# Performance work log

Hardware: AMD Instinct MI355X
Metric: run time of the kernel (lower is better)

Reference implementation:

```python
import jax, jax.numpy as jnp
import numpy as np

N_NODES = 100000

def _gcn_norm(edge_index, num_nodes):
    # PyG GCNConv: add self-loops, symmetric normalization deg^-1/2 A_hat deg^-1/2
    loop = jnp.arange(num_nodes, dtype=edge_index.dtype)
    src = jnp.concatenate([edge_index[0], loop])  # [E+N]
    dst = jnp.concatenate([edge_index[1], loop])  # [E+N]
    deg = jax.ops.segment_sum(jnp.ones(dst.shape[0], jnp.float32), dst, num_segments=num_nodes)
    dis = jnp.where(deg > 0, jax.lax.rsqrt(deg), 0.0)
    norm = dis[src] * dis[dst]  # [E+N]
    return src, dst, norm

def _gcn_layer(x, W, b, src, dst, norm, num_nodes):
    xw = x @ W                                   # [N, H] dense GEMM first (out_dim <= in_dim)
    msg = xw[src] * norm[:, None]                # gather + scale per edge
    out = jax.ops.segment_sum(msg, dst, num_segments=num_nodes)  # scatter-add
    return out + b

def setup_inputs() -> dict:
    key = jax.random.key(0)
    ks = jax.random.split(key, 6)
    E = 1600000
    return {
        "x": jax.random.normal(ks[0], (N_NODES, 512), jnp.float32),
        "edge_index": jax.random.randint(ks[1], (2, E), 0, N_NODES, dtype=jnp.int64),
        "W1": jax.random.normal(ks[2], (512, 256), jnp.float32) * 0.04,
        "b1": jnp.zeros((256,), jnp.float32),
        "W2": jax.random.normal(ks[3], (256, 256), jnp.float32) * 0.06,
        "b2": jnp.zeros((256,), jnp.float32),
        "fc_w": jax.random.normal(ks[4], (256, 128), jnp.float32) * 0.06,
        "fc_b": jnp.zeros((128,), jnp.float32),
    }

def reference(x, edge_index, W1, b1, W2, b2, fc_w, fc_b):
    src, dst, norm = _gcn_norm(edge_index, N_NODES)
    h = jax.nn.relu(_gcn_layer(x, W1, b1, src, dst, norm, N_NODES))
    h = jax.nn.relu(_gcn_layer(h, W2, b2, src, dst, norm, N_NODES))
    return h @ fc_w + fc_b
```

## Files before the change

### kernel.cpp

```cpp
#include <hip/hip_runtime.h>


#define N_NODES 100000
constexpr int D_IN  = 512;
constexpr int D_H   = 256;
constexpr int D_OUT = 128;
constexpr int M_PAD = 100096;

typedef _Float16 f16x8 __attribute__((ext_vector_type(8)));
typedef _Float16 f16x4 __attribute__((ext_vector_type(4)));
typedef float f32x4 __attribute__((ext_vector_type(4)));

#define GLD16(SRC, DST) __builtin_amdgcn_global_load_lds(                      \
    (const __attribute__((address_space(1))) void*)(SRC),                      \
    (__attribute__((address_space(3))) void*)(DST), 16, 0, 0)

__global__ __launch_bounds__(256) void cvt_x_k(const float* __restrict__ x,
                                               _Float16* __restrict__ x16) {
  size_t i = ((size_t)blockIdx.x * 256 + threadIdx.x) * 8;
  const size_t valid = (size_t)N_NODES * D_IN;
  if (i < valid) {
    float4 a = *(const float4*)(x + i);
    float4 b = *(const float4*)(x + i + 4);
    f16x8 v;
    v[0] = (_Float16)a.x; v[1] = (_Float16)a.y;
    v[2] = (_Float16)a.z; v[3] = (_Float16)a.w;
    v[4] = (_Float16)b.x; v[5] = (_Float16)b.y;
    v[6] = (_Float16)b.z; v[7] = (_Float16)b.w;
    *(f16x8*)(x16 + i) = v;
  } else if (i < (size_t)M_PAD * D_IN) {
    *(f16x8*)(x16 + i) = (f16x8){0, 0, 0, 0, 0, 0, 0, 0};
  }
}

__global__ __launch_bounds__(256) void deg_count_k(const int* __restrict__ dst,
                                                   int* __restrict__ deg,
                                                   int* __restrict__ pe, int E) {
  int i = (blockIdx.x * 256 + threadIdx.x) * 4;
  if (i + 3 < E) {
    int4 d = *(const int4*)(dst + i);
    int4 p;
    p.x = atomicAdd(&deg[d.x], 1);
    p.y = atomicAdd(&deg[d.y], 1);
    p.z = atomicAdd(&deg[d.z], 1);
    p.w = atomicAdd(&deg[d.w], 1);
    *(int4*)(pe + i) = p;
  } else {
    for (int t = i; t < E; ++t) pe[t] = atomicAdd(&deg[dst[t]], 1);
  }
}

__global__ __launch_bounds__(256) void scan1_k(const int* __restrict__ deg,
                                               int* __restrict__ off,
                                               int* __restrict__ bsum,
                                               float* __restrict__ dis, int n) {
  __shared__ int ts[256];
  const int tid = threadIdx.x;
  const int base = blockIdx.x * 1024 + tid * 4;
  int v[4];
#pragma unroll
  for (int t = 0; t < 4; ++t) v[t] = (base + t < n) ? deg[base + t] : 0;
#pragma unroll
  for (int t = 0; t < 4; ++t)
    if (base + t < n) dis[base + t] = rsqrtf((float)v[t] + 1.0f);
  const int tot = v[0] + v[1] + v[2] + v[3];
  ts[tid] = tot;
  __syncthreads();
  for (int o = 1; o < 256; o <<= 1) {
    int t = (tid >= o) ? ts[tid - o] : 0;
    __syncthreads();
    ts[tid] += t;
    __syncthreads();
  }
  int run = ts[tid] - tot;
#pragma unroll
  for (int t = 0; t < 4; ++t) {
    if (base + t < n) off[base + t] = run;
    run += v[t];
  }
  if (tid == 255) bsum[blockIdx.x] = ts[255];
}

__global__ __launch_bounds__(128) void scan2_k(int* __restrict__ bsum, int nb) {
  __shared__ int ts[128];
  const int tid = threadIdx.x;
  const int v = (tid < nb) ? bsum[tid] : 0;
  ts[tid] = v;
  __syncthreads();
  for (int o = 1; o < 128; o <<= 1) {
    int t = (tid >= o) ? ts[tid - o] : 0;
    __syncthreads();
    ts[tid] += t;
    __syncthreads();
  }
  if (tid < nb) bsum[tid] = ts[tid] - v;
}

__global__ __launch_bounds__(256) void fill_k(const int* __restrict__ src,
                                              const int* __restrict__ dst,
                                              const int* __restrict__ pe,
                                              const int* __restrict__ off,
                                              const int* __restrict__ bsum,
                                              int* __restrict__ ssorted, int E) {
  int i = (blockIdx.x * 256 + threadIdx.x) * 4;
  if (i + 3 < E) {
    int4 s = *(const int4*)(src + i);
    int4 d = *(const int4*)(dst + i);
    int4 p = *(const int4*)(pe + i);
    ssorted[off[d.x] + bsum[d.x >> 10] + p.x] = s.x;
    ssorted[off[d.y] + bsum[d.y >> 10] + p.y] = s.y;
    ssorted[off[d.z] + bsum[d.z >> 10] + p.z] = s.z;
    ssorted[off[d.w] + bsum[d.w >> 10] + p.w] = s.w;
  } else {
    for (int t = i; t < E; ++t) {
      int d = dst[t];
      ssorted[off[d] + bsum[d >> 10] + pe[t]] = src[t];
    }
  }
}

__global__ __launch_bounds__(256) void wtrans_all_k(const float* __restrict__ W1,
                                                    const float* __restrict__ W2,
                                                    const float* __restrict__ FC,
                                                    _Float16* __restrict__ w1t,
                                                    _Float16* __restrict__ w2t,
                                                    _Float16* __restrict__ fct) {
  int i = blockIdx.x * 256 + threadIdx.x;
  if (i < 131072) {
    int k = i >> 8, n = i & 255;
    w1t[(size_t)n * 512 + k] = (_Float16)W1[i];
  } else if (i < 196608) {
    int j = i - 131072;
    int k = j >> 8, n = j & 255;
    w2t[(size_t)n * 256 + k] = (_Float16)W2[j];
  } else if (i < 229376) {
    int j = i - 196608;
    int k = j >> 7, n = j & 127;
    fct[(size_t)n * 256 + k] = (_Float16)FC[j];
  }
}

template<int BN, bool OUT_Y>
__global__ __launch_bounds__(512, 4) void gemm_glds_k(
    const _Float16* __restrict__ A16,
    const _Float16* __restrict__ Bt,
    const float* __restrict__ bias,
    const float* __restrict__ dis,
    float* __restrict__ C,
    _Float16* __restrict__ Y,
    int M, int K) {
  constexpr int BM = 128, BK = 32;
  constexpr int FN  = BN / 64;
  constexpr int NBI = BN / 128;
  constexpr int ASZ = BM * BK;
  constexpr int BSZ = BN * BK;
  constexpr int EPAD = 4;

  __shared__ __align__(16) _Float16 smem[3 * (ASZ + BSZ)];
  _Float16* As = smem;
  _Float16* Bs = smem + 3 * ASZ;
  float* epi = (float*)smem;

  const int tid  = threadIdx.x;
  const int w    = tid >> 6, lane = tid & 63;
  const int wm   = w >> 2, wn = w & 3;
  const int l15  = lane & 15, l16 = lane >> 4;
  const int row0 = blockIdx.y * BM;

  const int lr = lane >> 2, lg = lane & 3;
  const int arow  = w * 16 + lr;
  const int brow0 = w * (NBI * 16) + lr;
  const int brow1 = brow0 + 16;
  const _Float16* srcA  = A16 + (size_t)(row0 + arow) * K + ((lg ^ (arow & 3)) << 3);
  const _Float16* srcB0 = Bt + (size_t)brow0 * K + ((lg ^ (brow0 & 3)) << 3);
  const _Float16* srcB1 = Bt + (size_t)brow1 * K + ((lg ^ (brow1 & 3)) << 3);
  _Float16* dstA  = &As[(w * 16) * BK];
  _Float16* dstB0 = &Bs[(w * (NBI * 16)) * BK];
  _Float16* dstB1 = &Bs[(w * (NBI * 16) + 16) * BK];

  f32x4 acc[4][FN];
#pragma unroll
  for (int i = 0; i < 4; ++i)
#pragma unroll
    for (int j = 0; j < FN; ++j) acc[i][j] = (f32x4){0.f, 0.f, 0.f, 0.f};

  const int nsteps = K >> 5;

  auto stage = [&](int t, int buf) {
    const int kt = t << 5;
    GLD16(srcA + kt, dstA + buf * ASZ);
    GLD16(srcB0 + kt, dstB0 + buf * BSZ);
    if constexpr (NBI == 2) GLD16(srcB1 + kt, dstB1 + buf * BSZ);
  };

  stage(0, 0);
  if (nsteps > 1) stage(1, 1);

  int rbuf = 0;
  int wbuf = 2;
  for (int t = 0; t < nsteps; ++t) {
    if (t + 1 < nsteps) {
      if constexpr (NBI == 2) asm volatile("s_waitcnt vmcnt(3)" ::: "memory");
      else                    asm volatile("s_waitcnt vmcnt(2)" ::: "memory");
    } else {
      asm volatile("s_waitcnt vmcnt(0)" ::: "memory");
    }
    __builtin_amdgcn_sched_barrier(0);
    __builtin_amdgcn_s_barrier();
    __builtin_amdgcn_sched_barrier(0);

    if (t + 2 < nsteps) stage(t + 2, wbuf);

    const _Float16* as = As + rbuf * ASZ;
    const _Float16* bs = Bs + rbuf * BSZ;
    f16x8 a[4], b[FN];
#pragma unroll
    for (int i = 0; i < 4; ++i) {
      const int r = wm * 64 + i * 16 + l15;
      a[i] = *(const f16x8*)&as[r * BK + ((l16 ^ (r & 3)) << 3)];
    }
#pragma unroll
    for (int j = 0; j < FN; ++j) {
      const int n = wn * (FN * 16) + j * 16 + l15;
      b[j] = *(const f16x8*)&bs[n * BK + ((l16 ^ (n & 3)) << 3)];
    }
#pragma unroll
    for (int i = 0; i < 4; ++i)
#pragma unroll
      for (int j = 0; j < FN; ++j)
        acc[i][j] = __builtin_amdgcn_mfma_f32_16x16x32_f16(a[i], b[j], acc[i][j], 0, 0, 0);

    rbuf = (rbuf == 2) ? 0 : rbuf + 1;
    wbuf = (wbuf == 2) ? 0 : wbuf + 1;
  }
  __syncthreads();

  constexpr int ESTR = BN + EPAD;
  constexpr int CPT  = BN / 16;
#pragma unroll
  for (int c = 0; c < 4; ++c) {
    if (wm == (c >> 1)) {
      const int ib = (c & 1) * 2;
#pragma unroll
      for (int ii = 0; ii < 2; ++ii) {
        const int i = ib + ii;
#pragma unroll
        for (int j = 0; j < FN; ++j) {
          const int col = wn * (FN * 16) + j * 16 + l15;
#pragma unroll
          for (int r = 0; r < 4; ++r) {
            const int lrow = ii * 16 + l16 * 4 + r;
            epi[lrow * ESTR + col] = acc[i][j][r];
          }
        }
      }
    }
    __syncthreads();
    {
      const int lrow = tid >> 4;
      const int grow = row0 + c * 32 + lrow;
      const int colb = (tid & 15) * CPT;
      if (grow < M) {
        float v[CPT];
#pragma unroll
        for (int q = 0; q < CPT; q += 4)
          *(float4*)&v[q] = *(const float4*)&epi[lrow * ESTR + colb + q];
        if constexpr (OUT_Y) {
          const float dv = dis[grow];
          f16x8 o[CPT / 8];
#pragma unroll
          for (int q = 0; q < CPT; ++q) o[q >> 3][q & 7] = (_Float16)(v[q] * dv);
#pragma unroll
          for (int q = 0; q < CPT / 8; ++q)
            *(f16x8*)(Y + (size_t)grow * BN + colb + q * 8) = o[q];
        } else {
#pragma unroll
          for (int q = 0; q < CPT; ++q) v[q] += bias[colb + q];
#pragma unroll
          for (int q = 0; q < CPT; q += 4)
            *(float4*)(C + (size_t)grow * BN + colb + q) = *(const float4*)&v[q];
        }
      }
    }
    __syncthreads();
  }
}

__global__ __launch_bounds__(256) void gather_k(const _Float16* __restrict__ y,
                                                const int* __restrict__ ssorted,
                                                const int* __restrict__ off,
                                                const int* __restrict__ bsum,
                                                const float* __restrict__ dis,
                                                const float* __restrict__ bias,
                                                _Float16* __restrict__ h,
                                                int n, int E) {
  const int gid = blockIdx.x * 256 + threadIdx.x;
  const int v = gid >> 6, lane = gid & 63;
  if (v >= n) return;

  const float dv = dis[v];
  const int fo = lane * 4;

  f16x4 sv = *(const f16x4*)(y + (size_t)v * 256 + fo);
  float4 acc = make_float4((float)sv[0], (float)sv[1], (float)sv[2], (float)sv[3]);

  const int beg = off[v] + bsum[v >> 10];
  const int end = (v + 1 < n) ? (off[v + 1] + bsum[(v + 1) >> 10]) : E;
  const int ne = end - beg;

  for (int j0 = 0; j0 < ne; j0 += 64) {
    const int rem = ne - j0;
    const int cnt = rem < 64 ? rem : 64;
    int s_l = 0;
    if (lane < cnt) s_l = ssorted[beg + j0 + lane];

    int k = 0;
    for (; k + 8 <= cnt; k += 8) {
      f16x4 yv[8];
#pragma unroll
      for (int u = 0; u < 8; ++u) {
        const int s = __shfl(s_l, k + u);
        yv[u] = *(const f16x4*)(y + (size_t)s * 256 + fo);
      }
#pragma unroll
      for (int u = 0; u < 8; ++u) {
        acc.x += (float)yv[u][0];
        acc.y += (float)yv[u][1];
        acc.z += (float)yv[u][2];
        acc.w += (float)yv[u][3];
      }
    }
    for (; k < cnt; ++k) {
      const int s = __shfl(s_l, k);
      const f16x4 yv = *(const f16x4*)(y + (size_t)s * 256 + fo);
      acc.x += (float)yv[0];
      acc.y += (float)yv[1];
      acc.z += (float)yv[2];
      acc.w += (float)yv[3];
    }
  }

  const float4 b = *(const float4*)(bias + fo);
  f16x4 o;
  o[0] = (_Float16)fmaxf(fmaf(dv, acc.x, b.x), 0.f);
  o[1] = (_Float16)fmaxf(fmaf(dv, acc.y, b.y), 0.f);
  o[2] = (_Float16)fmaxf(fmaf(dv, acc.z, b.z), 0.f);
  o[3] = (_Float16)fmaxf(fmaf(dv, acc.w, b.w), 0.f);
  *(f16x4*)(h + (size_t)v * 256 + fo) = o;
}

extern "C" void kernel_launch(void* const* d_in, const int* in_sizes, int n_in,
                              void* d_out, int out_size, void* d_ws, size_t ws_size,
                              hipStream_t stream) {
  const float* x    = (const float*)d_in[0];
  const int*   ei   = (const int*)d_in[1];
  const float* W1   = (const float*)d_in[2];
  const float* b1   = (const float*)d_in[3];
  const float* W2   = (const float*)d_in[4];
  const float* b2   = (const float*)d_in[5];
  const float* fc_w = (const float*)d_in[6];
  const float* fc_b = (const float*)d_in[7];
  float* out = (float*)d_out;

  const int E = in_sizes[1] / 2;
  const int* src = ei;
  const int* dst = ei + E;
  const int N = N_NODES;

  char* p = (char*)d_ws;
  int*   deg     = (int*)p;            p += (size_t)N * 4;
  float* dis     = (float*)p;          p += (size_t)N * 4;
  int*   off     = (int*)p;            p += (size_t)(N + 1) * 4;
  int*   pe      = (int*)p;            p += (size_t)E * 4;
  int*   ssorted = (int*)p;            p += (size_t)E * 4;
  int*   bsum    = (int*)p;            p += 512;
  p = (char*)(((size_t)p + 255) & ~(size_t)255);
  _Float16* w1t = (_Float16*)p;        p += (size_t)D_H   * D_IN * 2;
  _Float16* w2t = (_Float16*)p;        p += (size_t)D_H   * D_H  * 2;
  _Float16* fct = (_Float16*)p;        p += (size_t)D_OUT * D_H  * 2;
  p = (char*)(((size_t)p + 255) & ~(size_t)255);
  _Float16* x16 = (_Float16*)p;        p += (size_t)M_PAD * D_IN * 2;
  _Float16* y16 = (_Float16*)p;        p += (size_t)M_PAD * D_H * 2;
  _Float16* h16 = (_Float16*)p;        p += (size_t)M_PAD * D_H * 2;

  cvt_x_k<<<(M_PAD * (D_IN / 8) + 255) / 256, 256, 0, stream>>>(x, x16);
  wtrans_all_k<<<896, 256, 0, stream>>>(W1, W2, fc_w, w1t, w2t, fct);

  const int NB1 = (N + 1023) / 1024;
  const int EB4 = ((E + 3) / 4 + 255) / 256;
  hipMemsetAsync(deg, 0, N * sizeof(int), stream);
  deg_count_k<<<EB4, 256, 0, stream>>>(dst, deg, pe, E);
  scan1_k<<<NB1, 256, 0, stream>>>(deg, off, bsum, dis, N);
  scan2_k<<<1, 128, 0, stream>>>(bsum, NB1);
  fill_k<<<EB4, 256, 0, stream>>>(src, dst, pe, off, bsum, ssorted, E);

  const int node_wave_blocks = (N * 64 + 255) / 256;
  const dim3 gg(1, M_PAD / 128);

  gemm_glds_k<256, true><<<gg, 512, 0, stream>>>(
      x16, w1t, nullptr, dis, nullptr, y16, N, D_IN);
  gather_k<<<node_wave_blocks, 256, 0, stream>>>(y16, ssorted, off, bsum, dis, b1, h16, N, E);

  gemm_glds_k<256, true><<<gg, 512, 0, stream>>>(
      h16, w2t, nullptr, dis, nullptr, y16, N, D_H);
  gather_k<<<node_wave_blocks, 256, 0, stream>>>(y16, ssorted, off, bsum, dis, b2, h16, N, E);

  gemm_glds_k<128, false><<<gg, 512, 0, stream>>>(
      h16, fct, fc_b, nullptr, out, nullptr, N, D_H);
}
```

Before: 500.7 us.

## Fuse fp32-to-fp16 conversion of x into first GEMM's A-tile load

Drops the separate pass that converted x to fp16 and instead has the first GEMM stream fp32 A tiles directly into LDS, converting to fp16 when loading into registers. This removes one full write and re-read of a roughly 100 MB intermediate. In exchange the first GEMM moves twice the A bytes per tile, uses a double-buffered loop with a full barrier each step instead of the triple-buffered vmcnt pipeline, and adds per-fragment conversion work. The hipMemsetAsync on the degree array is also replaced with a small zeroing kernel.

```diff
diff --git a/kernel.cpp b/kernel.cpp
--- a/kernel.cpp
+++ b/kernel.cpp
@@ -15,21 +15,29 @@
     (const __attribute__((address_space(1))) void*)(SRC),                      \
     (__attribute__((address_space(3))) void*)(DST), 16, 0, 0)
 
-__global__ __launch_bounds__(256) void cvt_x_k(const float* __restrict__ x,
-                                               _Float16* __restrict__ x16) {
-  size_t i = ((size_t)blockIdx.x * 256 + threadIdx.x) * 8;
-  const size_t valid = (size_t)N_NODES * D_IN;
-  if (i < valid) {
-    float4 a = *(const float4*)(x + i);
-    float4 b = *(const float4*)(x + i + 4);
-    f16x8 v;
-    v[0] = (_Float16)a.x; v[1] = (_Float16)a.y;
-    v[2] = (_Float16)a.z; v[3] = (_Float16)a.w;
-    v[4] = (_Float16)b.x; v[5] = (_Float16)b.y;
-    v[6] = (_Float16)b.z; v[7] = (_Float16)b.w;
-    *(f16x8*)(x16 + i) = v;
-  } else if (i < (size_t)M_PAD * D_IN) {
-    *(f16x8*)(x16 + i) = (f16x8){0, 0, 0, 0, 0, 0, 0, 0};
+__global__ __launch_bounds__(256) void zero_deg_k(int* __restrict__ deg) {
+  int i = (blockIdx.x * 256 + threadIdx.x) * 4;
+  if (i < N_NODES) *(int4*)(deg + i) = make_int4(0, 0, 0, 0);
+}
+
+__global__ __launch_bounds__(256) void wtrans_k(const float* __restrict__ W1,
+                                                const float* __restrict__ W2,
+                                                const float* __restrict__ FC,
+                                                _Float16* __restrict__ w1t,
+                                                _Float16* __restrict__ w2t,
+                                                _Float16* __restrict__ fct) {
+  int i = blockIdx.x * 256 + threadIdx.x;
+  if (i < 131072) {
+    int k = i >> 8, n = i & 255;
+    w1t[(size_t)n * 512 + k] = (_Float16)W1[i];
+  } else if (i < 196608) {
+    int j = i - 131072;
+    int k = j >> 8, n = j & 255;
+    w2t[(size_t)n * 256 + k] = (_Float16)W2[j];
+  } else if (i < 229376) {
+    int j = i - 196608;
+    int k = j >> 7, n = j & 127;
+    fct[(size_t)n * 256 + k] = (_Float16)FC[j];
   }
 }
 
@@ -119,29 +127,9 @@
   }
 }
 
-__global__ __launch_bounds__(256) void wtrans_all_k(const float* __restrict__ W1,
-                                                    const float* __restrict__ W2,
-                                                    const float* __restrict__ FC,
-                                                    _Float16* __restrict__ w1t,
-                                                    _Float16* __restrict__ w2t,
-                                                    _Float16* __restrict__ fct) {
-  int i = blockIdx.x * 256 + threadIdx.x;
-  if (i < 131072) {
-    int k = i >> 8, n = i & 255;
-    w1t[(size_t)n * 512 + k] = (_Float16)W1[i];
-  } else if (i < 196608) {
-    int j = i - 131072;
-    int k = j >> 8, n = j & 255;
-    w2t[(size_t)n * 256 + k] = (_Float16)W2[j];
-  } else if (i < 229376) {
-    int j = i - 196608;
-    int k = j >> 7, n = j & 127;
-    fct[(size_t)n * 256 + k] = (_Float16)FC[j];
-  }
-}
-
-template<int BN, bool OUT_Y>
+template<int BN, bool AF32, bool OUT_Y>
 __global__ __launch_bounds__(512, 4) void gemm_glds_k(
+    const float* __restrict__ Af32,
     const _Float16* __restrict__ A16,
     const _Float16* __restrict__ Bt,
     const float* __restrict__ bias,
@@ -150,15 +138,15 @@
     _Float16* __restrict__ Y,
     int M, int K) {
   constexpr int BM = 128, BK = 32;
-  constexpr int FN  = BN / 64;
-  constexpr int NBI = BN / 128;
-  constexpr int ASZ = BM * BK;
-  constexpr int BSZ = BN * BK;
+  constexpr int FN   = BN / 64;
+  constexpr int NBI  = BN / 128;
+  constexpr int ASZ  = BM * BK;
+  constexpr int AFSZ = BM * BK;
+  constexpr int BSZ  = BN * BK;
   constexpr int EPAD = 4;
-
-  __shared__ __align__(16) _Float16 smem[3 * (ASZ + BSZ)];
-  _Float16* As = smem;
-  _Float16* Bs = smem + 3 * ASZ;
+  constexpr int SMEM_F16 = AF32 ? 2 * (2 * AFSZ + BSZ) : 3 * (ASZ + BSZ);
+
+  __shared__ __align__(16) _Float16 smem[SMEM_F16];
   float* epi = (float*)smem;
 
   const int tid  = threadIdx.x;
@@ -167,73 +155,131 @@
   const int l15  = lane & 15, l16 = lane >> 4;
   const int row0 = blockIdx.y * BM;
 
+  f32x4 acc[4][FN];
+#pragma unroll
+  for (int i = 0; i < 4; ++i)
+#pragma unroll
+    for (int j = 0; j < FN; ++j) acc[i][j] = (f32x4){0.f, 0.f, 0.f, 0.f};
+
+  const int nsteps = K >> 5;
+
   const int lr = lane >> 2, lg = lane & 3;
-  const int arow  = w * 16 + lr;
   const int brow0 = w * (NBI * 16) + lr;
   const int brow1 = brow0 + 16;
-  const _Float16* srcA  = A16 + (size_t)(row0 + arow) * K + ((lg ^ (arow & 3)) << 3);
   const _Float16* srcB0 = Bt + (size_t)brow0 * K + ((lg ^ (brow0 & 3)) << 3);
   const _Float16* srcB1 = Bt + (size_t)brow1 * K + ((lg ^ (brow1 & 3)) << 3);
-  _Float16* dstA  = &As[(w * 16) * BK];
-  _Float16* dstB0 = &Bs[(w * (NBI * 16)) * BK];
-  _Float16* dstB1 = &Bs[(w * (NBI * 16) + 16) * BK];
-
-  f32x4 acc[4][FN];
-#pragma unroll
-  for (int i = 0; i < 4; ++i)
-#pragma unroll
-    for (int j = 0; j < FN; ++j) acc[i][j] = (f32x4){0.f, 0.f, 0.f, 0.f};
-
-  const int nsteps = K >> 5;
-
-  auto stage = [&](int t, int buf) {
-    const int kt = t << 5;
-    GLD16(srcA + kt, dstA + buf * ASZ);
-    GLD16(srcB0 + kt, dstB0 + buf * BSZ);
-    if constexpr (NBI == 2) GLD16(srcB1 + kt, dstB1 + buf * BSZ);
-  };
-
-  stage(0, 0);
-  if (nsteps > 1) stage(1, 1);
-
-  int rbuf = 0;
-  int wbuf = 2;
-  for (int t = 0; t < nsteps; ++t) {
-    if (t + 1 < nsteps) {
-      if constexpr (NBI == 2) asm volatile("s_waitcnt vmcnt(3)" ::: "memory");
-      else                    asm volatile("s_waitcnt vmcnt(2)" ::: "memory");
-    } else {
-      asm volatile("s_waitcnt vmcnt(0)" ::: "memory");
-    }
-    __builtin_amdgcn_sched_barrier(0);
-    __builtin_amdgcn_s_barrier();
-    __builtin_amdgcn_sched_barrier(0);
-
-    if (t + 2 < nsteps) stage(t + 2, wbuf);
-
-    const _Float16* as = As + rbuf * ASZ;
-    const _Float16* bs = Bs + rbuf * BSZ;
-    f16x8 a[4], b[FN];
-#pragma unroll
-    for (int i = 0; i < 4; ++i) {
-      const int r = wm * 64 + i * 16 + l15;
-      a[i] = *(const f16x8*)&as[r * BK + ((l16 ^ (r & 3)) << 3)];
-    }
-#pragma unroll
-    for (int j = 0; j < FN; ++j) {
-      const int n = wn * (FN * 16) + j * 16 + l15;
-      b[j] = *(const f16x8*)&bs[n * BK + ((l16 ^ (n & 3)) << 3)];
-    }
-#pragma unroll
-    for (int i = 0; i < 4; ++i)
-#pragma unroll
-      for (int j = 0; j < FN; ++j)
-        acc[i][j] = __builtin_amdgcn_mfma_f32_16x16x32_f16(a[i], b[j], acc[i][j], 0, 0, 0);
-
-    rbuf = (rbuf == 2) ? 0 : rbuf + 1;
-    wbuf = (wbuf == 2) ? 0 : wbuf + 1;
-  }
-  __syncthreads();
+
+  if constexpr (AF32) {
+    float* Asf = (float*)smem;
+    _Float16* Bs = smem + 4 * AFSZ;
+    const int lr8 = lane >> 3, lg8 = lane & 7;
+    const int ar0 = w * 16 + lr8, ar1 = ar0 + 8;
+    int g0 = row0 + ar0; if (g0 >= M) g0 = M - 1;
+    int g1 = row0 + ar1; if (g1 >= M) g1 = M - 1;
+    const float* srcA0 = Af32 + (size_t)g0 * K + ((lg8 ^ (lr8 & 7)) << 2);
+    const float* srcA1 = Af32 + (size_t)g1 * K + ((lg8 ^ (lr8 & 7)) << 2);
+    float*    dA0 = Asf + (w * 16) * BK;
+    float*    dA1 = dA0 + 8 * BK;
+    _Float16* dB0 = &Bs[(w * (NBI * 16)) * BK];
+    _Float16* dB1 = &Bs[(w * (NBI * 16) + 16) * BK];
+
+    auto stage = [&](int t) {
+      const int kt = t << 5;
+      const int pa = (t & 1) * AFSZ, pb = (t & 1) * BSZ;
+      GLD16(srcA0 + kt, dA0 + pa);
+      GLD16(srcA1 + kt, dA1 + pa);
+      GLD16(srcB0 + kt, dB0 + pb);
+      if constexpr (NBI == 2) GLD16(srcB1 + kt, dB1 + pb);
+    };
+
+    stage(0);
+    __syncthreads();
+    for (int t = 0; t < nsteps; ++t) {
+      if (t + 1 < nsteps) stage(t + 1);
+      const float* as = Asf + (t & 1) * AFSZ;
+      const _Float16* bs = Bs + (t & 1) * BSZ;
+      f16x8 a[4], b[FN];
+#pragma unroll
+      for (int i = 0; i < 4; ++i) {
+        const int r = wm * 64 + i * 16 + l15;
+        const float* ar = as + r * BK;
+        const int s = r & 7;
+        float4 lo = *(const float4*)(ar + (((2 * l16) ^ s) << 2));
+        float4 hi = *(const float4*)(ar + (((2 * l16 + 1) ^ s) << 2));
+        a[i][0] = (_Float16)lo.x; a[i][1] = (_Float16)lo.y;
+        a[i][2] = (_Float16)lo.z; a[i][3] = (_Float16)lo.w;
+        a[i][4] = (_Float16)hi.x; a[i][5] = (_Float16)hi.y;
+        a[i][6] = (_Float16)hi.z; a[i][7] = (_Float16)hi.w;
+      }
+#pragma unroll
+      for (int j = 0; j < FN; ++j) {
+        const int n = wn * (FN * 16) + j * 16 + l15;
+        b[j] = *(const f16x8*)&bs[n * BK + ((l16 ^ (n & 3)) << 3)];
+      }
+#pragma unroll
+      for (int i = 0; i < 4; ++i)
+#pragma unroll
+        for (int j = 0; j < FN; ++j)
+          acc[i][j] = __builtin_amdgcn_mfma_f32_16x16x32_f16(a[i], b[j], acc[i][j], 0, 0, 0);
+      __syncthreads();
+    }
+  } else {
+    _Float16* As = smem;
+    _Float16* Bs = smem + 3 * ASZ;
+    const int arow = w * 16 + lr;
+    const _Float16* srcA = A16 + (size_t)(row0 + arow) * K + ((lg ^ (arow & 3)) << 3);
+    _Float16* dstA  = &As[(w * 16) * BK];
+    _Float16* dstB0 = &Bs[(w * (NBI * 16)) * BK];
+    _Float16* dstB1 = &Bs[(w * (NBI * 16) + 16) * BK];
+
+    auto stage = [&](int t, int buf) {
+      const int kt = t << 5;
+      GLD16(srcA + kt, dstA + buf * ASZ);
+      GLD16(srcB0 + kt, dstB0 + buf * BSZ);
+      if constexpr (NBI == 2) GLD16(srcB1 + kt, dstB1 + buf * BSZ);
+    };
+
+    stage(0, 0);
+    if (nsteps > 1) stage(1, 1);
+
+    int rbuf = 0, wbuf = 2;
+    for (int t = 0; t < nsteps; ++t) {
+      if (t + 1 < nsteps) {
+        if constexpr (NBI == 2) asm volatile("s_waitcnt vmcnt(3)" ::: "memory");
+        else                    asm volatile("s_waitcnt vmcnt(2)" ::: "memory");
+      } else {
+        asm volatile("s_waitcnt vmcnt(0)" ::: "memory");
+      }
+      __builtin_amdgcn_sched_barrier(0);
+      __builtin_amdgcn_s_barrier();
+      __builtin_amdgcn_sched_barrier(0);
+
+      if (t + 2 < nsteps) stage(t + 2, wbuf);
+
+      const _Float16* as = As + rbuf * ASZ;
+      const _Float16* bs = Bs + rbuf * BSZ;
+      f16x8 a[4], b[FN];
+#pragma unroll
+      for (int i = 0; i < 4; ++i) {
+        const int r = wm * 64 + i * 16 + l15;
+        a[i] = *(const f16x8*)&as[r * BK + ((l16 ^ (r & 3)) << 3)];
+      }
+#pragma unroll
+      for (int j = 0; j < FN; ++j) {
+        const int n = wn * (FN * 16) + j * 16 + l15;
+        b[j] = *(const f16x8*)&bs[n * BK + ((l16 ^ (n & 3)) << 3)];
+      }
+#pragma unroll
+      for (int i = 0; i < 4; ++i)
+#pragma unroll
+        for (int j = 0; j < FN; ++j)
+          acc[i][j] = __builtin_amdgcn_mfma_f32_16x16x32_f16(a[i], b[j], acc[i][j], 0, 0, 0);
+
+      rbuf = (rbuf == 2) ? 0 : rbuf + 1;
+      wbuf = (wbuf == 2) ? 0 : wbuf + 1;
+    }
+    __syncthreads();
+  }
 
   constexpr int ESTR = BN + EPAD;
   constexpr int CPT  = BN / 16;
@@ -379,16 +425,14 @@
   _Float16* w2t = (_Float16*)p;        p += (size_t)D_H   * D_H  * 2;
   _Float16* fct = (_Float16*)p;        p += (size_t)D_OUT * D_H  * 2;
   p = (char*)(((size_t)p + 255) & ~(size_t)255);
-  _Float16* x16 = (_Float16*)p;        p += (size_t)M_PAD * D_IN * 2;
   _Float16* y16 = (_Float16*)p;        p += (size_t)M_PAD * D_H * 2;
   _Float16* h16 = (_Float16*)p;        p += (size_t)M_PAD * D_H * 2;
 
-  cvt_x_k<<<(M_PAD * (D_IN / 8) + 255) / 256, 256, 0, stream>>>(x, x16);
-  wtrans_all_k<<<896, 256, 0, stream>>>(W1, W2, fc_w, w1t, w2t, fct);
+  wtrans_k<<<896, 256, 0, stream>>>(W1, W2, fc_w, w1t, w2t, fct);
+  zero_deg_k<<<(N / 4 + 255) / 256, 256, 0, stream>>>(deg);
 
   const int NB1 = (N + 1023) / 1024;
   const int EB4 = ((E + 3) / 4 + 255) / 256;
-  hipMemsetAsync(deg, 0, N * sizeof(int), stream);
   deg_count_k<<<EB4, 256, 0, stream>>>(dst, deg, pe, E);
   scan1_k<<<NB1, 256, 0, stream>>>(deg, off, bsum, dis, N);
   scan2_k<<<1, 128, 0, stream>>>(bsum, NB1);
@@ -397,14 +441,14 @@
   const int node_wave_blocks = (N * 64 + 255) / 256;
   const dim3 gg(1, M_PAD / 128);
 
-  gemm_glds_k<256, true><<<gg, 512, 0, stream>>>(
-      x16, w1t, nullptr, dis, nullptr, y16, N, D_IN);
+  gemm_glds_k<256, true, true><<<gg, 512, 0, stream>>>(
+      x, nullptr, w1t, nullptr, dis, nullptr, y16, N, D_IN);
   gather_k<<<node_wave_blocks, 256, 0, stream>>>(y16, ssorted, off, bsum, dis, b1, h16, N, E);
 
-  gemm_glds_k<256, true><<<gg, 512, 0, stream>>>(
-      h16, w2t, nullptr, dis, nullptr, y16, N, D_H);
+  gemm_glds_k<256, false, true><<<gg, 512, 0, stream>>>(
+      nullptr, h16, w2t, nullptr, dis, nullptr, y16, N, D_H);
   gather_k<<<node_wave_blocks, 256, 0, stream>>>(y16, ssorted, off, bsum, dis, b2, h16, N, E);
 
-  gemm_glds_k<128, false><<<gg, 512, 0, stream>>>(
-      h16, fct, fc_b, nullptr, out, nullptr, N, D_H);
-}
+  gemm_glds_k<128, false, false><<<gg, 512, 0, stream>>>(
+      nullptr, h16, fct, fc_b, nullptr, out, nullptr, N, D_H);
+}
```

Result: faster. 482.2 us (-3.7%).
